# Performance work log

Hardware: AMD Instinct MI355X
Metric: run time of the kernel (lower is better)

## Reference

```python
import jax, jax.numpy as jnp
import numpy as np

NEG_SLOPE = 0.01  # nn.LeakyReLU default


def setup_inputs() -> dict:
    key = jax.random.key(0)
    k1, k2, k3 = jax.random.split(key, 3)
    N, F_IN, F_OUT = 8192, 128, 64
    h = jax.random.normal(k1, (N, F_IN), dtype=jnp.float32)
    W = jax.random.normal(k2, (F_IN, F_OUT), dtype=jnp.float32) * (1.414 / np.sqrt(F_IN))
    a = jax.random.normal(k3, (2 * F_OUT, 1), dtype=jnp.float32) * (1.414 / np.sqrt(2 * F_OUT))
    return {"h": h, "W": W, "a": a}


def reference(h, W, a):
    # Wh: [N, F_out]
    Wh = h @ W
    F_out = W.shape[1]
    a1 = a[:F_out, 0]   # applies to the "source" (row) node i
    a2 = a[F_out:, 0]   # applies to the "target" (col) node j
    # e[i, j] = leakyrelu(a1 . Wh_i + a2 . Wh_j)  -- algebraic decomposition of
    # the concat-based score; avoids the O(N^2 * 2F) concat tensor.
    f1 = Wh @ a1  # [N]
    f2 = Wh @ a2  # [N]
    e = jax.nn.leaky_relu(f1[:, None] + f2[None, :], negative_slope=NEG_SLOPE)  # [N, N]
    attention = jax.nn.softmax(e, axis=1)
    # dropout is identity in eval mode (training=False)
    h_prime = attention @ Wh  # [N, F_out]
    return jax.nn.elu(h_prime)  # concat=True branch
```

## Files before the change

### kernel.cpp

```cpp
#include <hip/hip_runtime.h>
#include <hip/hip_bf16.h>
#include <stdint.h>

typedef float f32x4 __attribute__((ext_vector_type(4)));
typedef short s16x8 __attribute__((ext_vector_type(8)));
typedef unsigned int u32x4 __attribute__((ext_vector_type(4)));

#define L2E 1.44269504088896f

__device__ __forceinline__ unsigned short f2bf_rne(float f) {
    unsigned int u = __float_as_uint(f);
    u += 0x7fffu + ((u >> 16) & 1u);
    return (unsigned short)(u >> 16);
}

__global__ __launch_bounds__(256) void k1_wh(
    const float* __restrict__ hf,
    const float* __restrict__ Wf,
    const float* __restrict__ af,
    unsigned short* __restrict__ whB,
    float* __restrict__ f1L,
    float* __restrict__ f2L)
{
    __shared__ __align__(16) unsigned short Wt[64][136];
    __shared__ __align__(16) unsigned short tb[64][72];
    const int tid  = threadIdx.x;
    const int lane = tid & 63;
    const int w    = tid >> 6;
    const int col  = lane & 15;
    const int quad = lane >> 4;
    const int i0   = blockIdx.x * 64;

    #pragma unroll
    for (int it = 0; it < 8; ++it) {
        int fidx = tid + it * 256;
        int k  = fidx >> 4;
        int n4 = (fidx & 15) << 2;
        f32x4 wv = *(const f32x4*)&Wf[k * 64 + n4];
        #pragma unroll
        for (int e = 0; e < 4; ++e)
            Wt[n4 + e][k] = f2bf_rne(wv[e]);
    }
    __syncthreads();

    f32x4 D[4];
    #pragma unroll
    for (int f = 0; f < 4; ++f) D[f] = (f32x4){0.f, 0.f, 0.f, 0.f};

    const int rowA = i0 + w * 16 + col;
    #pragma unroll
    for (int cs = 0; cs < 4; ++cs) {
        f32x4 h0 = *(const f32x4*)&hf[(size_t)rowA * 128 + cs * 32 + quad * 8];
        f32x4 h1 = *(const f32x4*)&hf[(size_t)rowA * 128 + cs * 32 + quad * 8 + 4];
        s16x8 A;
        #pragma unroll
        for (int jj = 0; jj < 4; ++jj) {
            A[jj]     = (short)f2bf_rne(h0[jj]);
            A[4 + jj] = (short)f2bf_rne(h1[jj]);
        }
        #pragma unroll
        for (int f = 0; f < 4; ++f) {
            s16x8 B = *(const s16x8*)&Wt[f * 16 + col][cs * 32 + quad * 8];
            D[f] = __builtin_amdgcn_mfma_f32_16x16x32_bf16(A, B, D[f], 0, 0, 0);
        }
    }

    float a1v[4], a2v[4];
    #pragma unroll
    for (int f = 0; f < 4; ++f) {
        a1v[f] = af[f * 16 + col];
        a2v[f] = af[64 + f * 16 + col];
    }

    #pragma unroll
    for (int r = 0; r < 4; ++r) {
        float s1 = D[0][r]*a1v[0] + D[1][r]*a1v[1] + D[2][r]*a1v[2] + D[3][r]*a1v[3];
        float s2 = D[0][r]*a2v[0] + D[1][r]*a2v[1] + D[2][r]*a2v[2] + D[3][r]*a2v[3];
        #pragma unroll
        for (int d = 1; d < 16; d <<= 1) {
            s1 += __shfl_xor(s1, d, 64);
            s2 += __shfl_xor(s2, d, 64);
        }
        if (col == 0) {
            int i = i0 + w * 16 + quad * 4 + r;
            f1L[i] = s1 * L2E;
            f2L[i] = s2 * L2E;
        }
        #pragma unroll
        for (int f = 0; f < 4; ++f)
            tb[f * 16 + col][w * 16 + quad * 4 + r] = f2bf_rne(D[f][r]);
    }
    __syncthreads();

    for (int idx = tid; idx < 512; idx += 256) {
        int lane_o = idx & 63;
        int bq     = (idx >> 6) & 3;
        int jg_l   = idx >> 8;
        int col_o  = lane_o & 15, quad_o = lane_o >> 4;
        u32x4 v = *(const u32x4*)&tb[bq * 16 + col_o][jg_l * 32 + quad_o * 8];
        size_t off = (((size_t)((i0 >> 5) + jg_l) * 4 + bq) * 64 + lane_o) * 8;
        *(u32x4*)&whB[off] = v;
    }
}

__global__ __launch_bounds__(256) void k2_attn(
    const unsigned short* __restrict__ whB,
    const float* __restrict__ f1L,
    const float* __restrict__ f2L,
    float* __restrict__ Apart,
    float* __restrict__ rsumP)
{
    const int tid  = threadIdx.x;
    const int lane = tid & 63;
    const int w    = tid >> 6;
    const int col  = lane & 15;
    const int quad = lane >> 4;
    const int i0   = blockIdx.x * 64;
    const int jb   = blockIdx.y * 1024;

    const float f1 = f1L[i0 + w * 16 + col];

    f32x4 D0 = (f32x4){0.f,0.f,0.f,0.f}, D1 = D0, D2 = D0, D3 = D0, Ds = D0;
    s16x8 ones;
    #pragma unroll
    for (int jj = 0; jj < 8; ++jj) ones[jj] = (short)0x3f80;

    const unsigned short* bp = whB + ((size_t)(jb >> 5) * 256 + lane) * 8;

    #pragma unroll 2
    for (int jt = 0; jt < 32; ++jt) {
        const int jq = jb + jt * 32 + quad * 8;
        f32x4 fa = *(const f32x4*)&f2L[jq];
        f32x4 fb = *(const f32x4*)&f2L[jq + 4];
        const unsigned short* bb = bp + (size_t)jt * 2048;
        s16x8 B0 = *(const s16x8*)(bb);
        s16x8 B1 = *(const s16x8*)(bb + 512);
        s16x8 B2 = *(const s16x8*)(bb + 1024);
        s16x8 B3 = *(const s16x8*)(bb + 1536);
        unsigned int pb[8];
        #pragma unroll
        for (int e = 0; e < 4; ++e) {
            float u = f1 + fa[e];
            u = fmaxf(u, 0.01f * u);
            pb[e] = __float_as_uint(__builtin_amdgcn_exp2f(u));
            float v = f1 + fb[e];
            v = fmaxf(v, 0.01f * v);
            pb[4 + e] = __float_as_uint(__builtin_amdgcn_exp2f(v));
        }
        union { u32x4 u4; s16x8 s8; } Au;
        Au.u4[0] = __builtin_amdgcn_perm(pb[1], pb[0], 0x07060302u);
        Au.u4[1] = __builtin_amdgcn_perm(pb[3], pb[2], 0x07060302u);
        Au.u4[2] = __builtin_amdgcn_perm(pb[5], pb[4], 0x07060302u);
        Au.u4[3] = __builtin_amdgcn_perm(pb[7], pb[6], 0x07060302u);
        D0 = __builtin_amdgcn_mfma_f32_16x16x32_bf16(Au.s8, B0, D0, 0, 0, 0);
        D1 = __builtin_amdgcn_mfma_f32_16x16x32_bf16(Au.s8, B1, D1, 0, 0, 0);
        D2 = __builtin_amdgcn_mfma_f32_16x16x32_bf16(Au.s8, B2, D2, 0, 0, 0);
        D3 = __builtin_amdgcn_mfma_f32_16x16x32_bf16(Au.s8, B3, D3, 0, 0, 0);
        Ds = __builtin_amdgcn_mfma_f32_16x16x32_bf16(Au.s8, ones, Ds, 0, 0, 0);
    }

    float* Ap = Apart + (size_t)blockIdx.y * 524288;
    #pragma unroll
    for (int r = 0; r < 4; ++r) {
        int i = i0 + w * 16 + quad * 4 + r;
        Ap[(size_t)i * 64 +      col] = D0[r];
        Ap[(size_t)i * 64 + 16 + col] = D1[r];
        Ap[(size_t)i * 64 + 32 + col] = D2[r];
        Ap[(size_t)i * 64 + 48 + col] = D3[r];
        if (col == 0) rsumP[blockIdx.y * 8192 + i] = Ds[r];
    }
}

__global__ __launch_bounds__(256) void k3_combine(
    const float* __restrict__ Apart,
    const float* __restrict__ rsumP,
    float* __restrict__ out)
{
    int gid = blockIdx.x * 256 + threadIdx.x;
    int i  = gid >> 4;
    int c4 = (gid & 15) << 2;
    f32x4 num = (f32x4){0.f, 0.f, 0.f, 0.f};
    float den = 0.f;
    #pragma unroll
    for (int s = 0; s < 8; ++s) {
        num += *(const f32x4*)&Apart[(size_t)s * 524288 + (size_t)i * 64 + c4];
        den += rsumP[s * 8192 + i];
    }
    float rden = 1.f / den;
    f32x4 o;
    #pragma unroll
    for (int e = 0; e < 4; ++e) {
        float v = num[e] * rden;
        o[e] = v > 0.f ? v : (__builtin_amdgcn_exp2f(v * L2E) - 1.f);
    }
    *(f32x4*)&out[(size_t)i * 64 + c4] = o;
}

extern "C" void kernel_launch(void* const* d_in, const int* in_sizes, int n_in,
                              void* d_out, int out_size, void* d_ws, size_t ws_size,
                              hipStream_t stream) {
    const float* h = (const float*)d_in[0];
    const float* W = (const float*)d_in[1];
    const float* a = (const float*)d_in[2];
    float* out = (float*)d_out;

    char* ws = (char*)d_ws;
    unsigned short* whB = (unsigned short*)ws;
    float* f1L   = (float*)(ws + 1048576);
    float* f2L   = (float*)(ws + 1081344);
    float* Apart = (float*)(ws + 1114112);
    float* rsumP = (float*)(ws + 17891328);

    k1_wh<<<128, 256, 0, stream>>>(h, W, a, whB, f1L, f2L);
    k2_attn<<<dim3(128, 8), 256, 0, stream>>>(whB, f1L, f2L, Apart, rsumP);
    k3_combine<<<512, 256, 0, stream>>>(Apart, rsumP, out);
}
```

Baseline: 98.86 us.

## Fuse split-K combine into attention kernel via ticket counter and stage B in LDS

Removes the separate combine kernel: each attention block atomically increments a per-row-block counter, and the last of the eight split blocks sums the partial numerators and denominators, normalizes, and applies ELU. The counters are reset in the first kernel. The Wh tiles and f2 values are also staged through shared memory in chunks of 256 columns before the MFMA loop, instead of being read directly from global memory. This saves a launch and part of the partial-buffer traffic, at the cost of extra block syncs, a serialized tail in the last-arriving block, and more LDS use per block.

```diff
diff --git a/kernel.cpp b/kernel.cpp
--- a/kernel.cpp
+++ b/kernel.cpp
@@ -20,7 +20,8 @@
     const float* __restrict__ af,
     unsigned short* __restrict__ whB,
     float* __restrict__ f1L,
-    float* __restrict__ f2L)
+    float* __restrict__ f2L,
+    int* __restrict__ cnt)
 {
     __shared__ __align__(16) unsigned short Wt[64][136];
     __shared__ __align__(16) unsigned short tb[64][72];
@@ -31,6 +32,8 @@
     const int quad = lane >> 4;
     const int i0   = blockIdx.x * 64;
 
+    if (tid == 0) cnt[blockIdx.x] = 0;
+
     #pragma unroll
     for (int it = 0; it < 8; ++it) {
         int fidx = tid + it * 256;
@@ -108,15 +111,21 @@
     const float* __restrict__ f1L,
     const float* __restrict__ f2L,
     float* __restrict__ Apart,
-    float* __restrict__ rsumP)
+    float* __restrict__ rsumP,
+    int* __restrict__ cnt,
+    float* __restrict__ out)
 {
+    __shared__ __align__(16) unsigned short BtF[16384];
+    __shared__ __align__(16) float f2s[256];
+    __shared__ int ticket;
     const int tid  = threadIdx.x;
     const int lane = tid & 63;
     const int w    = tid >> 6;
     const int col  = lane & 15;
     const int quad = lane >> 4;
     const int i0   = blockIdx.x * 64;
-    const int jb   = blockIdx.y * 1024;
+    const int slot = blockIdx.y;
+    const int jb   = slot * 1024;
 
     const float f1 = f1L[i0 + w * 16 + col];
 
@@ -125,41 +134,53 @@
     #pragma unroll
     for (int jj = 0; jj < 8; ++jj) ones[jj] = (short)0x3f80;
 
-    const unsigned short* bp = whB + ((size_t)(jb >> 5) * 256 + lane) * 8;
-
-    #pragma unroll 2
-    for (int jt = 0; jt < 32; ++jt) {
-        const int jq = jb + jt * 32 + quad * 8;
-        f32x4 fa = *(const f32x4*)&f2L[jq];
-        f32x4 fb = *(const f32x4*)&f2L[jq + 4];
-        const unsigned short* bb = bp + (size_t)jt * 2048;
-        s16x8 B0 = *(const s16x8*)(bb);
-        s16x8 B1 = *(const s16x8*)(bb + 512);
-        s16x8 B2 = *(const s16x8*)(bb + 1024);
-        s16x8 B3 = *(const s16x8*)(bb + 1536);
-        unsigned int pb[8];
-        #pragma unroll
-        for (int e = 0; e < 4; ++e) {
-            float u = f1 + fa[e];
-            u = fmaxf(u, 0.01f * u);
-            pb[e] = __float_as_uint(__builtin_amdgcn_exp2f(u));
-            float v = f1 + fb[e];
-            v = fmaxf(v, 0.01f * v);
-            pb[4 + e] = __float_as_uint(__builtin_amdgcn_exp2f(v));
-        }
-        union { u32x4 u4; s16x8 s8; } Au;
-        Au.u4[0] = __builtin_amdgcn_perm(pb[1], pb[0], 0x07060302u);
-        Au.u4[1] = __builtin_amdgcn_perm(pb[3], pb[2], 0x07060302u);
-        Au.u4[2] = __builtin_amdgcn_perm(pb[5], pb[4], 0x07060302u);
-        Au.u4[3] = __builtin_amdgcn_perm(pb[7], pb[6], 0x07060302u);
-        D0 = __builtin_amdgcn_mfma_f32_16x16x32_bf16(Au.s8, B0, D0, 0, 0, 0);
-        D1 = __builtin_amdgcn_mfma_f32_16x16x32_bf16(Au.s8, B1, D1, 0, 0, 0);
-        D2 = __builtin_amdgcn_mfma_f32_16x16x32_bf16(Au.s8, B2, D2, 0, 0, 0);
-        D3 = __builtin_amdgcn_mfma_f32_16x16x32_bf16(Au.s8, B3, D3, 0, 0, 0);
-        Ds = __builtin_amdgcn_mfma_f32_16x16x32_bf16(Au.s8, ones, Ds, 0, 0, 0);
-    }
-
-    float* Ap = Apart + (size_t)blockIdx.y * 524288;
+    for (int s = 0; s < 4; ++s) {
+        __syncthreads();
+        if (tid < 64)
+            *(f32x4*)&f2s[tid * 4] = *(const f32x4*)&f2L[jb + (s << 8) + tid * 4];
+        {
+            const unsigned short* src = whB + ((size_t)(jb >> 5) + s * 8) * 2048;
+            #pragma unroll
+            for (int it = 0; it < 8; ++it) {
+                int idx = (tid + it * 256) * 8;
+                *(u32x4*)&BtF[idx] = *(const u32x4*)&src[idx];
+            }
+        }
+        __syncthreads();
+        #pragma unroll
+        for (int j0 = 0; j0 < 256; j0 += 32) {
+            const int jq = j0 + quad * 8;
+            f32x4 fa = *(const f32x4*)&f2s[jq];
+            f32x4 fb = *(const f32x4*)&f2s[jq + 4];
+            unsigned int pb[8];
+            #pragma unroll
+            for (int e = 0; e < 4; ++e) {
+                float u = f1 + fa[e];
+                u = fmaxf(u, 0.01f * u);
+                pb[e] = __float_as_uint(__builtin_amdgcn_exp2f(u));
+                float v = f1 + fb[e];
+                v = fmaxf(v, 0.01f * v);
+                pb[4 + e] = __float_as_uint(__builtin_amdgcn_exp2f(v));
+            }
+            union { u32x4 u4; s16x8 s8; } Au;
+            Au.u4[0] = __builtin_amdgcn_perm(pb[1], pb[0], 0x07060302u);
+            Au.u4[1] = __builtin_amdgcn_perm(pb[3], pb[2], 0x07060302u);
+            Au.u4[2] = __builtin_amdgcn_perm(pb[5], pb[4], 0x07060302u);
+            Au.u4[3] = __builtin_amdgcn_perm(pb[7], pb[6], 0x07060302u);
+            const unsigned short* bf = &BtF[(size_t)(j0 >> 5) * 2048 + lane * 8];
+            s16x8 B0 = *(const s16x8*)(bf);
+            s16x8 B1 = *(const s16x8*)(bf + 512);
+            s16x8 B2 = *(const s16x8*)(bf + 1024);
+            s16x8 B3 = *(const s16x8*)(bf + 1536);
+            D0 = __builtin_amdgcn_mfma_f32_16x16x32_bf16(Au.s8, B0, D0, 0, 0, 0);
+            D1 = __builtin_amdgcn_mfma_f32_16x16x32_bf16(Au.s8, B1, D1, 0, 0, 0);
+            D2 = __builtin_amdgcn_mfma_f32_16x16x32_bf16(Au.s8, B2, D2, 0, 0, 0);
+            D3 = __builtin_amdgcn_mfma_f32_16x16x32_bf16(Au.s8, B3, D3, 0, 0, 0);
+            Ds = __builtin_amdgcn_mfma_f32_16x16x32_bf16(Au.s8, ones, Ds, 0, 0, 0);
+        }
+    }
+
+    float* Ap = Apart + (size_t)slot * 524288;
     #pragma unroll
     for (int r = 0; r < 4; ++r) {
         int i = i0 + w * 16 + quad * 4 + r;
@@ -167,33 +188,43 @@
         Ap[(size_t)i * 64 + 16 + col] = D1[r];
         Ap[(size_t)i * 64 + 32 + col] = D2[r];
         Ap[(size_t)i * 64 + 48 + col] = D3[r];
-        if (col == 0) rsumP[blockIdx.y * 8192 + i] = Ds[r];
-    }
-}
-
-__global__ __launch_bounds__(256) void k3_combine(
-    const float* __restrict__ Apart,
-    const float* __restrict__ rsumP,
-    float* __restrict__ out)
-{
-    int gid = blockIdx.x * 256 + threadIdx.x;
-    int i  = gid >> 4;
-    int c4 = (gid & 15) << 2;
-    f32x4 num = (f32x4){0.f, 0.f, 0.f, 0.f};
-    float den = 0.f;
-    #pragma unroll
-    for (int s = 0; s < 8; ++s) {
-        num += *(const f32x4*)&Apart[(size_t)s * 524288 + (size_t)i * 64 + c4];
-        den += rsumP[s * 8192 + i];
-    }
-    float rden = 1.f / den;
-    f32x4 o;
-    #pragma unroll
-    for (int e = 0; e < 4; ++e) {
-        float v = num[e] * rden;
-        o[e] = v > 0.f ? v : (__builtin_amdgcn_exp2f(v * L2E) - 1.f);
-    }
-    *(f32x4*)&out[(size_t)i * 64 + c4] = o;
+        if (col == 0) rsumP[slot * 8192 + i] = Ds[r];
+    }
+
+    __threadfence();
+    __syncthreads();
+    if (tid == 0) ticket = atomicAdd(&cnt[blockIdx.x], 1);
+    __syncthreads();
+    if (ticket != 7) return;
+    __threadfence();
+
+    #pragma unroll
+    for (int r = 0; r < 4; ++r) {
+        int i = i0 + w * 16 + quad * 4 + r;
+        float den = Ds[r];
+        float num0 = D0[r], num1 = D1[r], num2 = D2[r], num3 = D3[r];
+        #pragma unroll
+        for (int s = 0; s < 8; ++s) {
+            if (s == slot) continue;
+            den  += rsumP[s * 8192 + i];
+            const float* As = Apart + (size_t)s * 524288 + (size_t)i * 64;
+            num0 += As[     col];
+            num1 += As[16 + col];
+            num2 += As[32 + col];
+            num3 += As[48 + col];
+        }
+        float rden = 1.f / den;
+        float v0 = num0 * rden, v1 = num1 * rden;
+        float v2 = num2 * rden, v3 = num3 * rden;
+        v0 = v0 > 0.f ? v0 : (__builtin_amdgcn_exp2f(v0 * L2E) - 1.f);
+        v1 = v1 > 0.f ? v1 : (__builtin_amdgcn_exp2f(v1 * L2E) - 1.f);
+        v2 = v2 > 0.f ? v2 : (__builtin_amdgcn_exp2f(v2 * L2E) - 1.f);
+        v3 = v3 > 0.f ? v3 : (__builtin_amdgcn_exp2f(v3 * L2E) - 1.f);
+        out[(size_t)i * 64 +      col] = v0;
+        out[(size_t)i * 64 + 16 + col] = v1;
+        out[(size_t)i * 64 + 32 + col] = v2;
+        out[(size_t)i * 64 + 48 + col] = v3;
+    }
 }
 
 extern "C" void kernel_launch(void* const* d_in, const int* in_sizes, int n_in,
@@ -208,10 +239,10 @@
     unsigned short* whB = (unsigned short*)ws;
     float* f1L   = (float*)(ws + 1048576);
     float* f2L   = (float*)(ws + 1081344);
-    float* Apart = (float*)(ws + 1114112);
-    float* rsumP = (float*)(ws + 17891328);
-
-    k1_wh<<<128, 256, 0, stream>>>(h, W, a, whB, f1L, f2L);
-    k2_attn<<<dim3(128, 8), 256, 0, stream>>>(whB, f1L, f2L, Apart, rsumP);
-    k3_combine<<<512, 256, 0, stream>>>(Apart, rsumP, out);
-}
+    int*   cnt   = (int*)  (ws + 1114112);
+    float* Apart = (float*)(ws + 1114624);
+    float* rsumP = (float*)(ws + 17891840);
+
+    k1_wh<<<128, 256, 0, stream>>>(h, W, a, whB, f1L, f2L, cnt);
+    k2_attn<<<dim3(128, 8), 256, 0, stream>>>(whB, f1L, f2L, Apart, rsumP, cnt, out);
+}
```

Result: slower. 215.8 us (+118.3%).
